# Kernel tuning notes

Hardware: AMD Instinct MI355X
Metric: run time of the kernel (lower is better)

The kernel has to match this reference:

```python
import jax, jax.numpy as jnp
import numpy as np

VOC_SIZE = 512
CHAR_EMB = 128
N_FILT = 16
KERNELS = [2, 3, 4, 5, 6]
PADS = [0, 0, 1, 2, 3]
B, L = 16384, 32


def _conv1d(x, w, b, pad):
    # x: [B, C, L], w: [O, I, K] -> [B, O, L_out]
    y = jax.lax.conv_general_dilated(
        x, w, window_strides=(1,), padding=[(pad, pad)],
        dimension_numbers=("NCH", "OIH", "NCH"))
    return y + b[None, :, None]


def setup_inputs() -> dict:
    key = jax.random.key(0)
    ks = jax.random.split(key, 12)
    word = jax.random.randint(ks[0], (B, L), 0, VOC_SIZE, dtype=jnp.int64 if jax.config.jax_enable_x64 else jnp.int32)
    emb = jax.random.normal(ks[1], (VOC_SIZE, CHAR_EMB), dtype=jnp.float32) * 0.1
    inp = {"word": word, "emb": emb}
    for i, k in enumerate(KERNELS):
        fan_in = CHAR_EMB * k
        bound = 1.0 / np.sqrt(fan_in)
        inp[f"w{k}"] = jax.random.uniform(ks[2 + 2 * i], (N_FILT, CHAR_EMB, k), jnp.float32, -bound, bound)
        inp[f"b{k}"] = jax.random.uniform(ks[3 + 2 * i], (N_FILT,), jnp.float32, -bound, bound)
    return inp


def reference(word, emb, w2, b2, w3, b3, w4, b4, w5, b5, w6, b6):
    unk = word < 0                      # [B, L]
    idx = jnp.where(unk, 0, word)
    x = emb[idx]                        # [B, L, E]
    x = jnp.where(unk[..., None], 0.0, x)
    x = jnp.transpose(x, (0, 2, 1))     # [B, E, L]
    ws = [w2, w3, w4, w5, w6]
    bs = [b2, b3, b4, b5, b6]
    maxima = [jnp.max(_conv1d(x, w, b, p), axis=-1)
              for w, b, p in zip(ws, bs, PADS)]  # each [B, 16]
    return jnp.concatenate(maxima, axis=-1)      # [B, 80]
```

## Files before the change

### kernel.cpp

```cpp
#include <hip/hip_runtime.h>
#include <hip/hip_fp16.h>
#include <math.h>

#define VOC      512
#define EMB      128
#define L_SEQ    32
#define NWORDS   16384
#define NCOL     416
#define WPB      128
#define SCPITCH  129

__device__ __constant__ int SEGBASE_H[5] = {0, 16416, 49248, 82080, 147744};
__device__ __constant__ int SEGW_H[5]    = {32, 64, 64, 128, 128};

__global__ __launch_bounds__(NCOL) void pack_wt(
    const float* __restrict__ w2, const float* __restrict__ w3,
    const float* __restrict__ w4, const float* __restrict__ w5,
    const float* __restrict__ w6,
    float* __restrict__ wt)
{
    const int i   = blockIdx.x;
    const int col = threadIdx.x;

    int k, jpad, base; const float* w;
    if (col < 32)       { k = 2; jpad = 2; base = 0;   w = w2; }
    else if (col < 96)  { k = 3; jpad = 4; base = 32;  w = w3; }
    else if (col < 160) { k = 4; jpad = 4; base = 96;  w = w4; }
    else if (col < 288) { k = 5; jpad = 8; base = 160; w = w5; }
    else                { k = 6; jpad = 8; base = 288; w = w6; }

    const int r  = col - base;
    const int ol = (jpad == 2) ? (r >> 1) : (jpad == 4) ? (r >> 2) : (r >> 3);
    const int j  = r & (jpad - 1);

    wt[i * NCOL + col] = (j < k) ? w[(ol * EMB + i) * k + j] : 0.f;
}

__device__ __forceinline__ void col_map(int col, int& seg, int& local) {
    if (col < 32)       { seg = 0; local = col; }
    else if (col < 96)  { seg = 1; local = col - 32; }
    else if (col < 160) { seg = 2; local = col - 96; }
    else if (col < 288) { seg = 3; local = col - 160; }
    else                { seg = 4; local = col - 288; }
}

__global__ __launch_bounds__(512) void build_pe16(
    const float* __restrict__ emb,
    const float* __restrict__ wt,
    __half* __restrict__ pe)
{
    const int c   = blockIdx.x;
    const int tid = threadIdx.x;

    if (c == VOC) {
        if (tid < NCOL) {
            int seg, local; col_map(tid, seg, local);
            pe[SEGBASE_H[seg] + VOC * SEGW_H[seg] + local] = __float2half(0.f);
        }
        return;
    }

    __shared__ float e[EMB];
    if (tid < EMB) e[tid] = emb[c * EMB + tid];
    __syncthreads();
    if (tid >= NCOL) return;

    float s = 0.f;
    #pragma unroll 8
    for (int i = 0; i < EMB; ++i) s += e[i] * wt[i * NCOL + tid];

    int seg, local; col_map(tid, seg, local);
    pe[SEGBASE_H[seg] + c * SEGW_H[seg] + local] = __float2half(s);
}

__device__ __forceinline__ float2 h2tof2(int u) {
    return __half22float2(__builtin_bit_cast(__half2, u));
}

template<int K> struct LdT;
template<> struct LdT<2> { using T = int;  };
template<> struct LdT<3> { using T = int2; };
template<> struct LdT<4> { using T = int2; };
template<> struct LdT<5> { using T = int4; };
template<> struct LdT<6> { using T = int4; };

template<int K>
__device__ __forceinline__ void unpack(typename LdT<K>::T q, float* v) {
    if constexpr (K == 2) {
        float2 f = h2tof2(q); v[0] = f.x; v[1] = f.y;
    } else if constexpr (K == 3) {
        float2 f0 = h2tof2(q.x), f1 = h2tof2(q.y);
        v[0] = f0.x; v[1] = f0.y; v[2] = f1.x;
    } else if constexpr (K == 4) {
        float2 f0 = h2tof2(q.x), f1 = h2tof2(q.y);
        v[0] = f0.x; v[1] = f0.y; v[2] = f1.x; v[3] = f1.y;
    } else if constexpr (K == 5) {
        float2 f0 = h2tof2(q.x), f1 = h2tof2(q.y), f2 = h2tof2(q.z);
        v[0] = f0.x; v[1] = f0.y; v[2] = f1.x; v[3] = f1.y; v[4] = f2.x;
    } else {
        float2 f0 = h2tof2(q.x), f1 = h2tof2(q.y), f2 = h2tof2(q.z);
        v[0] = f0.x; v[1] = f0.y; v[2] = f1.x; v[3] = f1.y;
        v[4] = f2.x; v[5] = f2.y;
    }
}

template<int K, int PAD, int LANEB>
__device__ __forceinline__ float convseg(const char* __restrict__ tab,
                                         const int* __restrict__ sc,
                                         int w, int ol, float bias)
{
    using LT = typename LdT<K>::T;
    constexpr int LOUT = L_SEQ + 2 * PAD - K + 1;
    const int lb = ol * LANEB;

    float s[LOUT];
    #pragma unroll
    for (int t = 0; t < LOUT; ++t) s[t] = bias;

    #pragma unroll
    for (int g = 0; g < 4; ++g) {
        int off[8];
        #pragma unroll
        for (int u = 0; u < 8; ++u)
            off[u] = sc[(g * 8 + u) * SCPITCH + w] + lb;
        LT q[8];
        #pragma unroll
        for (int u = 0; u < 8; ++u)
            q[u] = *(const LT*)(tab + off[u]);
        #pragma unroll
        for (int u = 0; u < 8; ++u) {
            const int tp = g * 8 + u;
            float v[K];
            unpack<K>(q[u], v);
            #pragma unroll
            for (int j = 0; j < K; ++j) {
                int t = tp + PAD - j;
                if (t >= 0 && t < LOUT) s[t] += v[j];
            }
        }
    }

    float m = s[0];
    #pragma unroll
    for (int t = 1; t < LOUT; ++t) m = fmaxf(m, s[t]);
    return m;
}

__global__ __launch_bounds__(1024) void conv_max(
    const int*    __restrict__ word,
    const __half* __restrict__ pe,
    const float* __restrict__ b2, const float* __restrict__ b3,
    const float* __restrict__ b4, const float* __restrict__ b5,
    const float* __restrict__ b6,
    float*       __restrict__ out)
{
    __shared__ __align__(16) __half tab[65664];
    __shared__ int sc[L_SEQ * SCPITCH];

    const int tid   = threadIdx.x;
    const int seg   = blockIdx.x % 5;
    const int wb    = blockIdx.x / 5;
    const int wbase = wb * WPB;

    const int segwH = SEGW_H[seg];
    const int nI4   = (513 * segwH) >> 3;

    const int4* src = (const int4*)(pe + SEGBASE_H[seg]);
    int4* dst = (int4*)tab;
    for (int i = tid; i < nI4; i += 1024) dst[i] = src[i];

    const int segwB = segwH * 2;
    #pragma unroll
    for (int r = 0; r < 4; ++r) {
        int i = tid + r * 1024;
        int c = word[wbase * L_SEQ + i];
        int w = i >> 5, tp = i & 31;
        sc[tp * SCPITCH + w] = (c >= 0 ? c : VOC) * segwB;
    }
    __syncthreads();

    const int ol = tid & 15;
    const int w0 = tid >> 4;
    const float* bp;
    switch (seg) {
        case 0:  bp = b2; break; case 1: bp = b3; break;
        case 2:  bp = b4; break; case 3: bp = b5; break;
        default: bp = b6; break;
    }
    const float bias = bp[ol];
    const char* tb = (const char*)tab;

    float m0, m1;
    switch (seg) {
        case 0:  m0 = convseg<2, 0, 4 >(tb, sc, w0,      ol, bias);
                 m1 = convseg<2, 0, 4 >(tb, sc, w0 + 64, ol, bias); break;
        case 1:  m0 = convseg<3, 0, 8 >(tb, sc, w0,      ol, bias);
                 m1 = convseg<3, 0, 8 >(tb, sc, w0 + 64, ol, bias); break;
        case 2:  m0 = convseg<4, 1, 8 >(tb, sc, w0,      ol, bias);
                 m1 = convseg<4, 1, 8 >(tb, sc, w0 + 64, ol, bias); break;
        case 3:  m0 = convseg<5, 2, 16>(tb, sc, w0,      ol, bias);
                 m1 = convseg<5, 2, 16>(tb, sc, w0 + 64, ol, bias); break;
        default: m0 = convseg<6, 3, 16>(tb, sc, w0,      ol, bias);
                 m1 = convseg<6, 3, 16>(tb, sc, w0 + 64, ol, bias); break;
    }
    out[(wbase + w0     ) * 80 + seg * 16 + ol] = m0;
    out[(wbase + w0 + 64) * 80 + seg * 16 + ol] = m1;
}

extern "C" void kernel_launch(void* const* d_in, const int* in_sizes, int n_in,
                              void* d_out, int out_size, void* d_ws, size_t ws_size,
                              hipStream_t stream)
{
    const int*   word = (const int*)  d_in[0];
    const float* emb  = (const float*)d_in[1];
    const float* w2   = (const float*)d_in[2];
    const float* b2   = (const float*)d_in[3];
    const float* w3   = (const float*)d_in[4];
    const float* b3   = (const float*)d_in[5];
    const float* w4   = (const float*)d_in[6];
    const float* b4   = (const float*)d_in[7];
    const float* w5   = (const float*)d_in[8];
    const float* b5   = (const float*)d_in[9];
    const float* w6   = (const float*)d_in[10];
    const float* b6   = (const float*)d_in[11];
    float* out = (float*)d_out;

    __half* pe16 = (__half*)d_ws;
    float*  wt   = (float*)((char*)d_ws + 430080);

    pack_wt<<<EMB, NCOL, 0, stream>>>(w2, w3, w4, w5, w6, wt);

    build_pe16<<<VOC + 1, 512, 0, stream>>>(emb, wt, pe16);

    conv_max<<<5 * (NWORDS / WPB), 1024, 0, stream>>>(
        word, pe16, b2, b3, b4, b5, b6, out);
}
```

Before: 106.8 us.

## Split conv segments into half-filter sub-blocks and fuse weight packing into table build

The conv kernel now splits each filter-size segment into two 8-filter halves, so each block copies a smaller projected-embedding table into shared memory (at most 513x64 halves instead of 513x128). This shrinks LDS use per block and allows 512-thread blocks with up to 4 blocks per CU. Word indices are stored as 16-bit pre-shifted offsets in a word-major layout and read as int4 vectors, replacing 32 scalar shared loads per word. The pack_wt kernel is removed and build_pe computes four vocabulary rows per block directly from the raw weights, saving one launch. In exchange, the per-word index staging and table copy are repeated across twice as many blocks.

```diff
diff --git a/kernel.cpp b/kernel.cpp
--- a/kernel.cpp
+++ b/kernel.cpp
@@ -1,6 +1,5 @@
 #include <hip/hip_runtime.h>
 #include <hip/hip_fp16.h>
-#include <math.h>
 
 #define VOC      512
 #define EMB      128
@@ -8,69 +7,62 @@
 #define NWORDS   16384
 #define NCOL     416
 #define WPB      128
-#define SCPITCH  129
-
-__device__ __constant__ int SEGBASE_H[5] = {0, 16416, 49248, 82080, 147744};
-__device__ __constant__ int SEGW_H[5]    = {32, 64, 64, 128, 128};
-
-__global__ __launch_bounds__(NCOL) void pack_wt(
+#define SCP      48
+
+__device__ __constant__ int SUBBASE[10] = {0, 8208, 16416, 32832, 49248,
+                                           65664, 82080, 114912, 147744, 180576};
+__device__ __constant__ int SUBW[10]    = {16, 16, 32, 32, 32, 32, 64, 64, 64, 64};
+
+__global__ __launch_bounds__(512) void build_pe(
+    const float* __restrict__ emb,
     const float* __restrict__ w2, const float* __restrict__ w3,
     const float* __restrict__ w4, const float* __restrict__ w5,
     const float* __restrict__ w6,
-    float* __restrict__ wt)
-{
-    const int i   = blockIdx.x;
-    const int col = threadIdx.x;
-
-    int k, jpad, base; const float* w;
-    if (col < 32)       { k = 2; jpad = 2; base = 0;   w = w2; }
-    else if (col < 96)  { k = 3; jpad = 4; base = 32;  w = w3; }
-    else if (col < 160) { k = 4; jpad = 4; base = 96;  w = w4; }
-    else if (col < 288) { k = 5; jpad = 8; base = 160; w = w5; }
-    else                { k = 6; jpad = 8; base = 288; w = w6; }
-
-    const int r  = col - base;
-    const int ol = (jpad == 2) ? (r >> 1) : (jpad == 4) ? (r >> 2) : (r >> 3);
-    const int j  = r & (jpad - 1);
-
-    wt[i * NCOL + col] = (j < k) ? w[(ol * EMB + i) * k + j] : 0.f;
-}
-
-__device__ __forceinline__ void col_map(int col, int& seg, int& local) {
-    if (col < 32)       { seg = 0; local = col; }
-    else if (col < 96)  { seg = 1; local = col - 32; }
-    else if (col < 160) { seg = 2; local = col - 96; }
-    else if (col < 288) { seg = 3; local = col - 160; }
-    else                { seg = 4; local = col - 288; }
-}
-
-__global__ __launch_bounds__(512) void build_pe16(
-    const float* __restrict__ emb,
-    const float* __restrict__ wt,
     __half* __restrict__ pe)
 {
-    const int c   = blockIdx.x;
+    __shared__ float e[4][EMB];
     const int tid = threadIdx.x;
-
-    if (c == VOC) {
-        if (tid < NCOL) {
-            int seg, local; col_map(tid, seg, local);
-            pe[SEGBASE_H[seg] + VOC * SEGW_H[seg] + local] = __float2half(0.f);
+    const int c0  = blockIdx.x * 4;
+    {
+        const int ch = tid >> 7, i = tid & 127;
+        const int c  = c0 + ch;
+        e[ch][i] = (c < VOC) ? emb[c * EMB + i] : 0.f;
+    }
+    __syncthreads();
+
+    const int col = tid;
+    if (col >= NCOL) return;
+
+    int k, jpad, base, seg; const float* w;
+    if (col < 32)       { k = 2; jpad = 2; base = 0;   seg = 0; w = w2; }
+    else if (col < 96)  { k = 3; jpad = 4; base = 32;  seg = 1; w = w3; }
+    else if (col < 160) { k = 4; jpad = 4; base = 96;  seg = 2; w = w4; }
+    else if (col < 288) { k = 5; jpad = 8; base = 160; seg = 3; w = w5; }
+    else                { k = 6; jpad = 8; base = 288; seg = 4; w = w6; }
+
+    const int r   = col - base;
+    const int ol  = (jpad == 2) ? (r >> 1) : (jpad == 4) ? (r >> 2) : (r >> 3);
+    const int j   = r & (jpad - 1);
+    const int sub = seg * 2 + (ol >> 3);
+    const int loc = (ol & 7) * jpad + j;
+
+    float a0 = 0.f, a1 = 0.f, a2 = 0.f, a3 = 0.f;
+    if (j < k) {
+        const float* wp = w + (ol * EMB) * k + j;
+        #pragma unroll 8
+        for (int i = 0; i < EMB; ++i) {
+            const float wv = wp[i * k];
+            a0 += wv * e[0][i]; a1 += wv * e[1][i];
+            a2 += wv * e[2][i]; a3 += wv * e[3][i];
         }
-        return;
-    }
-
-    __shared__ float e[EMB];
-    if (tid < EMB) e[tid] = emb[c * EMB + tid];
-    __syncthreads();
-    if (tid >= NCOL) return;
-
-    float s = 0.f;
-    #pragma unroll 8
-    for (int i = 0; i < EMB; ++i) s += e[i] * wt[i * NCOL + tid];
-
-    int seg, local; col_map(tid, seg, local);
-    pe[SEGBASE_H[seg] + c * SEGW_H[seg] + local] = __float2half(s);
+    }
+    const int W = SUBW[sub], Bb = SUBBASE[sub];
+    const float a[4] = {a0, a1, a2, a3};
+    #pragma unroll
+    for (int ch = 0; ch < 4; ++ch) {
+        const int c = c0 + ch;
+        if (c <= VOC) pe[Bb + c * W + loc] = __float2half(a[ch]);
+    }
 }
 
 __device__ __forceinline__ float2 h2tof2(int u) {
@@ -105,13 +97,19 @@
 }
 
 template<int K, int PAD, int LANEB>
-__device__ __forceinline__ float convseg(const char* __restrict__ tab,
-                                         const int* __restrict__ sc,
-                                         int w, int ol, float bias)
+__device__ __forceinline__ float convseg(
+    const char* __restrict__ tb, const unsigned short* __restrict__ sc,
+    int w, int lb, float bias)
 {
     using LT = typename LdT<K>::T;
     constexpr int LOUT = L_SEQ + 2 * PAD - K + 1;
-    const int lb = ol * LANEB;
+
+    int4 s4[4];
+    {
+        const int4* sp = (const int4*)(sc + w * SCP);
+        #pragma unroll
+        for (int g = 0; g < 4; ++g) s4[g] = sp[g];
+    }
 
     float s[LOUT];
     #pragma unroll
@@ -119,14 +117,14 @@
 
     #pragma unroll
     for (int g = 0; g < 4; ++g) {
-        int off[8];
-        #pragma unroll
-        for (int u = 0; u < 8; ++u)
-            off[u] = sc[(g * 8 + u) * SCPITCH + w] + lb;
+        const int dd[4] = {s4[g].x, s4[g].y, s4[g].z, s4[g].w};
         LT q[8];
         #pragma unroll
-        for (int u = 0; u < 8; ++u)
-            q[u] = *(const LT*)(tab + off[u]);
+        for (int u = 0; u < 8; ++u) {
+            const int pm = (u & 1) ? (int)(((unsigned)dd[u >> 1]) >> 16)
+                                   : (dd[u >> 1] & 0xffff);
+            q[u] = *(const LT*)(tb + (pm << 1) + lb);
+        }
         #pragma unroll
         for (int u = 0; u < 8; ++u) {
             const int tp = g * 8 + u;
@@ -134,7 +132,7 @@
             unpack<K>(q[u], v);
             #pragma unroll
             for (int j = 0; j < K; ++j) {
-                int t = tp + PAD - j;
+                const int t = tp + PAD - j;
                 if (t >= 0 && t < LOUT) s[t] += v[j];
             }
         }
@@ -146,7 +144,7 @@
     return m;
 }
 
-__global__ __launch_bounds__(1024) void conv_max(
+__global__ __launch_bounds__(512, 4) void conv_max(
     const int*    __restrict__ word,
     const __half* __restrict__ pe,
     const float* __restrict__ b2, const float* __restrict__ b3,
@@ -154,57 +152,54 @@
     const float* __restrict__ b6,
     float*       __restrict__ out)
 {
-    __shared__ __align__(16) __half tab[65664];
-    __shared__ int sc[L_SEQ * SCPITCH];
-
-    const int tid   = threadIdx.x;
-    const int seg   = blockIdx.x % 5;
-    const int wb    = blockIdx.x / 5;
-    const int wbase = wb * WPB;
-
-    const int segwH = SEGW_H[seg];
-    const int nI4   = (513 * segwH) >> 3;
-
-    const int4* src = (const int4*)(pe + SEGBASE_H[seg]);
+    __shared__ __align__(16) __half tab[513 * 64];
+    __shared__ __align__(16) unsigned short sc16[WPB * SCP];
+
+    const int tid  = threadIdx.x;
+    const int sub  = blockIdx.x % 10;
+    const int wb   = blockIdx.x / 10;
+    const int seg  = sub >> 1;
+    const int half = sub & 1;
+
+    const int  W16 = SUBW[sub];
+    const int  nI4 = (513 * W16) >> 3;
+    const int4* src = (const int4*)(pe + SUBBASE[sub]);
     int4* dst = (int4*)tab;
-    for (int i = tid; i < nI4; i += 1024) dst[i] = src[i];
-
-    const int segwB = segwH * 2;
-    #pragma unroll
-    for (int r = 0; r < 4; ++r) {
-        int i = tid + r * 1024;
-        int c = word[wbase * L_SEQ + i];
-        int w = i >> 5, tp = i & 31;
-        sc[tp * SCPITCH + w] = (c >= 0 ? c : VOC) * segwB;
+    for (int i = tid; i < nI4; i += 512) dst[i] = src[i];
+
+    const int shb = (seg == 0) ? 4 : (seg <= 2) ? 5 : 6;
+    #pragma unroll
+    for (int r = 0; r < 8; ++r) {
+        const int i  = tid + r * 512;
+        const int c  = word[wb * (WPB * L_SEQ) + i];
+        const int ce = (c >= 0) ? c : VOC;
+        sc16[(i >> 5) * SCP + (i & 31)] = (unsigned short)(ce << shb);
     }
     __syncthreads();
 
-    const int ol = tid & 15;
-    const int w0 = tid >> 4;
-    const float* bp;
-    switch (seg) {
-        case 0:  bp = b2; break; case 1: bp = b3; break;
-        case 2:  bp = b4; break; case 3: bp = b5; break;
-        default: bp = b6; break;
-    }
-    const float bias = bp[ol];
+    const int ol = tid & 7;
+    const int w0 = tid >> 3;
+    const float* bp = (seg == 0) ? b2 : (seg == 1) ? b3 :
+                      (seg == 2) ? b4 : (seg == 3) ? b5 : b6;
+    const float bias = bp[half * 8 + ol];
     const char* tb = (const char*)tab;
 
     float m0, m1;
     switch (seg) {
-        case 0:  m0 = convseg<2, 0, 4 >(tb, sc, w0,      ol, bias);
-                 m1 = convseg<2, 0, 4 >(tb, sc, w0 + 64, ol, bias); break;
-        case 1:  m0 = convseg<3, 0, 8 >(tb, sc, w0,      ol, bias);
-                 m1 = convseg<3, 0, 8 >(tb, sc, w0 + 64, ol, bias); break;
-        case 2:  m0 = convseg<4, 1, 8 >(tb, sc, w0,      ol, bias);
-                 m1 = convseg<4, 1, 8 >(tb, sc, w0 + 64, ol, bias); break;
-        case 3:  m0 = convseg<5, 2, 16>(tb, sc, w0,      ol, bias);
-                 m1 = convseg<5, 2, 16>(tb, sc, w0 + 64, ol, bias); break;
-        default: m0 = convseg<6, 3, 16>(tb, sc, w0,      ol, bias);
-                 m1 = convseg<6, 3, 16>(tb, sc, w0 + 64, ol, bias); break;
-    }
-    out[(wbase + w0     ) * 80 + seg * 16 + ol] = m0;
-    out[(wbase + w0 + 64) * 80 + seg * 16 + ol] = m1;
+        case 0:  m0 = convseg<2, 0, 4 >(tb, sc16, w0,      ol * 4,  bias);
+                 m1 = convseg<2, 0, 4 >(tb, sc16, w0 + 64, ol * 4,  bias); break;
+        case 1:  m0 = convseg<3, 0, 8 >(tb, sc16, w0,      ol * 8,  bias);
+                 m1 = convseg<3, 0, 8 >(tb, sc16, w0 + 64, ol * 8,  bias); break;
+        case 2:  m0 = convseg<4, 1, 8 >(tb, sc16, w0,      ol * 8,  bias);
+                 m1 = convseg<4, 1, 8 >(tb, sc16, w0 + 64, ol * 8,  bias); break;
+        case 3:  m0 = convseg<5, 2, 16>(tb, sc16, w0,      ol * 16, bias);
+                 m1 = convseg<5, 2, 16>(tb, sc16, w0 + 64, ol * 16, bias); break;
+        default: m0 = convseg<6, 3, 16>(tb, sc16, w0,      ol * 16, bias);
+                 m1 = convseg<6, 3, 16>(tb, sc16, w0 + 64, ol * 16, bias); break;
+    }
+    const int oc = seg * 16 + half * 8 + ol;
+    out[(wb * WPB + w0     ) * 80 + oc] = m0;
+    out[(wb * WPB + w0 + 64) * 80 + oc] = m1;
 }
 
 extern "C" void kernel_launch(void* const* d_in, const int* in_sizes, int n_in,
@@ -226,12 +221,9 @@
     float* out = (float*)d_out;
 
     __half* pe16 = (__half*)d_ws;
-    float*  wt   = (float*)((char*)d_ws + 430080);
-
-    pack_wt<<<EMB, NCOL, 0, stream>>>(w2, w3, w4, w5, w6, wt);
-
-    build_pe16<<<VOC + 1, 512, 0, stream>>>(emb, wt, pe16);
-
-    conv_max<<<5 * (NWORDS / WPB), 1024, 0, stream>>>(
+
+    build_pe<<<129, 512, 0, stream>>>(emb, w2, w3, w4, w5, w6, pe16);
+
+    conv_max<<<10 * (NWORDS / WPB), 512, 0, stream>>>(
         word, pe16, b2, b3, b4, b5, b6, out);
 }
```

After: 103.6 us. -3.0%, faster.
